# Optimization experiments

Hardware: AMD Instinct MI355X
Metric: run time of the kernel (lower is better)

The kernel has to match this reference:

```python
import jax, jax.numpy as jnp
import numpy as np

# dims
B, N, D, H, L = 2, 4096, 768, 12, 2
DH = D // H          # 64, equals BigBird block_size
BS = 64              # block size
NB = N // BS         # 64 blocks
R = 3                # num_random_blocks
FF = 4 * D
EPS = 1e-12          # BigBird layer_norm_eps


def _ln(x, g, b):
    mu = jnp.mean(x, -1, keepdims=True)
    var = jnp.mean(jnp.square(x - mu), -1, keepdims=True)
    return (x - mu) * jax.lax.rsqrt(var + EPS) * g + b


def _gelu_new(x):
    c = np.sqrt(2.0 / np.pi).astype(np.float32)
    return 0.5 * x * (1.0 + jnp.tanh(c * (x + 0.044715 * x * x * x)))


def _block_sparse_attn(q, k, v, rb):
    # q,k,v: [B,H,N,DH]; rb: [H,NB,R] random block ids (constant)
    scale = 1.0 / np.sqrt(DH).astype(np.float32)
    qb = q.reshape(B, H, NB, BS, DH)
    kb = k.reshape(B, H, NB, BS, DH)
    vb = v.reshape(B, H, NB, BS, DH)
    M = NB - 2
    mids = jnp.arange(1, NB - 1)
    win = jnp.stack([mids - 1, mids, mids + 1], -1)                    # [M,3]
    glb = jnp.broadcast_to(jnp.array([0, NB - 1], jnp.int32), (M, 2))  # [M,2]
    idx = jnp.concatenate([
        jnp.broadcast_to(glb[None], (H, M, 2)),
        jnp.broadcast_to(win[None], (H, M, 3)),
        rb[:, 1:NB - 1, :]], axis=-1)                                  # [H,M,8]
    hh = jnp.arange(H)[:, None, None]
    # gather key/value blocks: [B,H,M,8,BS,DH] -> [B,H,M,512,DH]
    kg = kb[:, hh, idx].reshape(B, H, M, -1, DH)
    vg = vb[:, hh, idx].reshape(B, H, M, -1, DH)
    qm = qb[:, :, 1:NB - 1]                                            # [B,H,M,BS,DH]
    s = jnp.einsum('bhmqd,bhmkd->bhmqk', qm, kg) * scale
    cm = jnp.einsum('bhmqk,bhmkd->bhmqd', jax.nn.softmax(s, -1), vg)
    # first and last query blocks attend globally (full attention)
    qe = jnp.stack([qb[:, :, 0], qb[:, :, -1]], 2)                     # [B,H,2,BS,DH]
    se = jnp.einsum('bheqd,bhkd->bheqk', qe, k) * scale
    ce = jnp.einsum('bheqk,bhkd->bheqd', jax.nn.softmax(se, -1), v)
    out = jnp.concatenate([ce[:, :, :1], cm, ce[:, :, 1:]], axis=2)    # [B,H,NB,BS,DH]
    return out.reshape(B, H, N, DH)


def _forward(inputs_embeds, rand_blocks, pos_emb, tt_emb, emb_ln_g, emb_ln_b,
             Wq, bq, Wk, bk, Wv, bv, Wo, bo, ln1_g, ln1_b,
             Wi, bi, Wd, bd, ln2_g, ln2_b, fc_w, fc_b):
    x = inputs_embeds + pos_emb[None] + tt_emb                         # embeddings (token_type id 0)
    x = _ln(x, emb_ln_g, emb_ln_b)
    for l in range(L):
        q = (x @ Wq[l] + bq[l]).reshape(B, N, H, DH).transpose(0, 2, 1, 3)
        k = (x @ Wk[l] + bk[l]).reshape(B, N, H, DH).transpose(0, 2, 1, 3)
        v = (x @ Wv[l] + bv[l]).reshape(B, N, H, DH).transpose(0, 2, 1, 3)
        ctx = _block_sparse_attn(q, k, v, rand_blocks[l])
        ctx = ctx.transpose(0, 2, 1, 3).reshape(B, N, D)
        a = _ln(x + ctx @ Wo[l] + bo[l], ln1_g[l], ln1_b[l])
        h = _gelu_new(a @ Wi[l] + bi[l])
        x = _ln(a + h @ Wd[l] + bd[l], ln2_g[l], ln2_b[l])
    pooled = jnp.mean(x, axis=1)                                       # [B,D]; dropout is identity at eval
    return (pooled @ fc_w + fc_b).squeeze()                            # [B]


def setup_inputs() -> dict:
    key = jax.random.key(0)
    ks = jax.random.split(key, 24)
    s = 0.02
    nrm = lambda k, shp: jax.random.normal(k, shp, jnp.float32) * s
    return {
        'inputs_embeds': jax.random.normal(ks[0], (B, N, D), jnp.float32),
        'rand_blocks': jax.random.randint(ks[1], (L, H, NB, R), 0, NB, jnp.int32),
        'pos_emb': nrm(ks[2], (N, D)),
        'tt_emb': nrm(ks[3], (D,)),
        'emb_ln_g': jnp.ones((D,), jnp.float32), 'emb_ln_b': jnp.zeros((D,), jnp.float32),
        'Wq': nrm(ks[4], (L, D, D)), 'bq': jnp.zeros((L, D), jnp.float32),
        'Wk': nrm(ks[5], (L, D, D)), 'bk': jnp.zeros((L, D), jnp.float32),
        'Wv': nrm(ks[6], (L, D, D)), 'bv': jnp.zeros((L, D), jnp.float32),
        'Wo': nrm(ks[7], (L, D, D)), 'bo': jnp.zeros((L, D), jnp.float32),
        'ln1_g': jnp.ones((L, D), jnp.float32), 'ln1_b': jnp.zeros((L, D), jnp.float32),
        'Wi': nrm(ks[8], (L, D, FF)), 'bi': jnp.zeros((L, FF), jnp.float32),
        'Wd': nrm(ks[9], (L, FF, D)), 'bd': jnp.zeros((L, D), jnp.float32),
        'ln2_g': jnp.ones((L, D), jnp.float32), 'ln2_b': jnp.zeros((L, D), jnp.float32),
        'fc_w': nrm(ks[10], (D, 1)), 'fc_b': jnp.zeros((1,), jnp.float32),
    }


def reference(inputs_embeds, rand_blocks, pos_emb, tt_emb, emb_ln_g, emb_ln_b,
              Wq, bq, Wk, bk, Wv, bv, Wo, bo, ln1_g, ln1_b,
              Wi, bi, Wd, bd, ln2_g, ln2_b, fc_w, fc_b):
    return _forward(inputs_embeds, rand_blocks, pos_emb, tt_emb, emb_ln_g, emb_ln_b,
                    Wq, bq, Wk, bk, Wv, bv, Wo, bo, ln1_g, ln1_b,
                    Wi, bi, Wd, bd, ln2_g, ln2_b, fc_w, fc_b)
```

## Files before the change

kernel.cpp:

```cpp
#include <hip/hip_runtime.h>
#include <math.h>

#define B_ 2
#define N_ 4096
#define D_ 768
#define H_ 12
#define DH_ 64
#define NB_ 64
#define FF_ 3072
#define LAYERS_ 2
#define ROWS_ (B_ * N_)

typedef __attribute__((ext_vector_type(8))) short s16x8;
typedef __attribute__((ext_vector_type(8))) unsigned short u16x8;
typedef __attribute__((ext_vector_type(4))) float f32x4;

typedef const __attribute__((address_space(1))) unsigned int ga_u32;
typedef __attribute__((address_space(3))) unsigned int lds_u32;

static __device__ __forceinline__ float gelu_fast(float x) {
    float z2 = 1.5957691216057308f * x * (1.0f + 0.044715f * x * x);
    return x * __builtin_amdgcn_rcpf(1.0f + __expf(-z2));
}

static __device__ __forceinline__ unsigned bf16_rne(float f) {
    unsigned u = __float_as_uint(f);
    return (u + 0x7FFFu + ((u >> 16) & 1u)) >> 16;
}
static __device__ __forceinline__ float bfh2f(unsigned short h) {
    return __uint_as_float(((unsigned)h) << 16);
}

__global__ __launch_bounds__(256)
void prep_weights(const float* __restrict__ Wq, const float* __restrict__ Wk,
                  const float* __restrict__ Wv, const float* __restrict__ Wo,
                  const float* __restrict__ Wi, const float* __restrict__ Wd,
                  unsigned short* __restrict__ Wt) {
    const size_t LW = 7077888;
    int bid = blockIdx.x;
    int l = bid / 1728, r = bid % 1728;
    const float* W; unsigned short* T; int K, N, t, nx;
    if (r < 576) {
        int which = r / 144; t = r % 144; nx = 12; K = 768; N = 768;
        W = (which == 0 ? Wq : which == 1 ? Wk : which == 2 ? Wv : Wo) + (size_t)l * D_ * D_;
        T = Wt + l * LW + (size_t)(which < 3 ? which * 768 * 768 : 2304 * 768);
    } else if (r < 1152) {
        t = r - 576; nx = 48; K = 768; N = 3072;
        W = Wi + (size_t)l * D_ * FF_;
        T = Wt + l * LW + (size_t)(2304 * 768 + 768 * 768);
    } else {
        t = r - 1152; nx = 12; K = 3072; N = 768;
        W = Wd + (size_t)l * FF_ * D_;
        T = Wt + l * LW + (size_t)(2304 * 768 + 768 * 768 + 3072 * 768);
    }
    const int bx = t % nx, by = t / nx;
    __shared__ unsigned short tile[64][72];
    const int k0 = by * 64, n0 = bx * 64;
    const int tt = threadIdx.x;
    const int rr = tt >> 2, c0 = (tt & 3) * 16;
    const float* src = W + (size_t)(k0 + rr) * N + n0 + c0;
#pragma unroll
    for (int j = 0; j < 4; ++j) {
        float4 v = *(const float4*)(src + j * 4);
        tile[rr][c0 + j * 4 + 0] = (unsigned short)bf16_rne(v.x);
        tile[rr][c0 + j * 4 + 1] = (unsigned short)bf16_rne(v.y);
        tile[rr][c0 + j * 4 + 2] = (unsigned short)bf16_rne(v.z);
        tile[rr][c0 + j * 4 + 3] = (unsigned short)bf16_rne(v.w);
    }
    __syncthreads();
    const int nr = tt >> 2, kc = (tt & 3) * 16;
    unsigned short* dst = T + (size_t)(n0 + nr) * K + k0 + kc;
    ushort4 o;
#pragma unroll
    for (int j = 0; j < 4; ++j) {
        o.x = tile[kc + j * 4 + 0][nr];
        o.y = tile[kc + j * 4 + 1][nr];
        o.z = tile[kc + j * 4 + 2][nr];
        o.w = tile[kc + j * 4 + 3][nr];
        *(ushort4*)(dst + j * 4) = o;
    }
}

template <int OMODE>
__global__ __launch_bounds__(256)
void gemm_bt(const unsigned short* __restrict__ A, const unsigned short* __restrict__ Bt,
             const float* __restrict__ bias, void* __restrict__ Cv,
             int N, int K, int gelu) {
    __shared__ __align__(16) unsigned short smem[17408];
    const int tid = threadIdx.x, lane = tid & 63, wid = tid >> 6;
    const int bid = blockIdx.x;
    const int row0 = (bid & 63) * 128, col0 = (bid >> 6) * 128;
    const int rh = (wid >> 1) * 64, ch = (wid & 1) * 64;
    const int fr = lane & 15, fq = lane >> 4;
    const int srow = wid * 32 + (lane >> 2);
    const int skoff = ((lane & 3) ^ ((lane >> 3) & 3)) * 8;
    const unsigned short* gA0 = A + (size_t)(row0 + srow) * K + skoff;
    const unsigned short* gA1 = gA0 + (size_t)16 * K;
    const unsigned short* gB0 = Bt + (size_t)(col0 + srow) * K + skoff;
    const unsigned short* gB1 = gB0 + (size_t)16 * K;
    const int rdo = (fq ^ ((fr >> 1) & 3)) * 8;

    f32x4 acc[4][4] = {};
    const int nk = K >> 5;
    {
        unsigned short* s = smem;
        __builtin_amdgcn_global_load_lds((ga_u32*)gA0, (lds_u32*)&s[wid * 1024], 16, 0, 0);
        __builtin_amdgcn_global_load_lds((ga_u32*)gA1, (lds_u32*)&s[wid * 1024 + 512], 16, 0, 0);
        __builtin_amdgcn_global_load_lds((ga_u32*)gB0, (lds_u32*)&s[4096 + wid * 1024], 16, 0, 0);
        __builtin_amdgcn_global_load_lds((ga_u32*)gB1, (lds_u32*)&s[4096 + wid * 1024 + 512], 16, 0, 0);
    }
    for (int kt = 0; kt < nk; ++kt) {
        __syncthreads();
        if (kt + 1 < nk) {
            int k0 = (kt + 1) << 5;
            unsigned short* s = smem + ((kt + 1) & 1) * 8192;
            __builtin_amdgcn_global_load_lds((ga_u32*)(gA0 + k0), (lds_u32*)&s[wid * 1024], 16, 0, 0);
            __builtin_amdgcn_global_load_lds((ga_u32*)(gA1 + k0), (lds_u32*)&s[wid * 1024 + 512], 16, 0, 0);
            __builtin_amdgcn_global_load_lds((ga_u32*)(gB0 + k0), (lds_u32*)&s[4096 + wid * 1024], 16, 0, 0);
            __builtin_amdgcn_global_load_lds((ga_u32*)(gB1 + k0), (lds_u32*)&s[4096 + wid * 1024 + 512], 16, 0, 0);
        }
        const unsigned short* sA = smem + (kt & 1) * 8192;
        const unsigned short* sB = sA + 4096;
        s16x8 af[4], bf[4];
#pragma unroll
        for (int i = 0; i < 4; ++i)
            af[i] = *(const s16x8*)&sA[(rh + 16 * i + fr) * 32 + rdo];
#pragma unroll
        for (int j = 0; j < 4; ++j)
            bf[j] = *(const s16x8*)&sB[(ch + 16 * j + fr) * 32 + rdo];
#pragma unroll
        for (int i = 0; i < 4; ++i)
#pragma unroll
            for (int j = 0; j < 4; ++j)
                acc[i][j] = __builtin_amdgcn_mfma_f32_16x16x32_bf16(af[i], bf[j], acc[i][j], 0, 0, 0);
    }
    if (OMODE == 0) {
#pragma unroll
        for (int j = 0; j < 4; ++j) {
            int col = col0 + ch + 16 * j + fr;
            float bb = bias[col];
#pragma unroll
            for (int i = 0; i < 4; ++i)
#pragma unroll
                for (int r = 0; r < 4; ++r) {
                    int row = row0 + rh + 16 * i + fq * 4 + r;
                    float v = acc[i][j][r] + bb;
                    if (gelu) v = gelu_fast(v);
                    ((float*)Cv)[(size_t)row * N + col] = v;
                }
        }
    } else {
        unsigned short* sC = smem;
        __syncthreads();
#pragma unroll
        for (int j = 0; j < 4; ++j) {
            float bb = bias[col0 + ch + 16 * j + fr];
#pragma unroll
            for (int i = 0; i < 4; ++i)
#pragma unroll
                for (int r = 0; r < 4; ++r) {
                    float v = acc[i][j][r] + bb;
                    if (gelu) v = gelu_fast(v);
                    sC[(rh + 16 * i + fq * 4 + r) * 136 + ch + 16 * j + fr] =
                        (unsigned short)bf16_rne(v);
                }
        }
        __syncthreads();
#pragma unroll
        for (int p = 0; p < 8; ++p) {
            int seg = p * 256 + tid;
            int r = seg >> 4, c8 = (seg & 15) * 8;
            *(u16x8*)&((unsigned short*)Cv)[(size_t)(row0 + r) * N + col0 + c8] =
                *(const u16x8*)&sC[r * 136 + c8];
        }
    }
}

__global__ __launch_bounds__(256)
void gemm_qkv(const unsigned short* __restrict__ A, const unsigned short* __restrict__ Bt,
              const float* __restrict__ bq, const float* __restrict__ bk,
              const float* __restrict__ bv,
              unsigned short* __restrict__ Qh, unsigned short* __restrict__ Kh,
              unsigned short* __restrict__ VT) {
    const int K = D_;
    __shared__ __align__(16) unsigned short smem[17408];
    const int tid = threadIdx.x, lane = tid & 63, wid = tid >> 6;
    const int bid = blockIdx.x;
    const int row0 = (bid & 63) * 128;
    const int bx = bid >> 6;
    const int col0 = bx * 128;
    const int rh = (wid >> 1) * 64, ch = (wid & 1) * 64;
    const int fr = lane & 15, fq = lane >> 4;
    const int srow = wid * 32 + (lane >> 2);
    const int skoff = ((lane & 3) ^ ((lane >> 3) & 3)) * 8;
    const unsigned short* gA0 = A + (size_t)(row0 + srow) * K + skoff;
    const unsigned short* gA1 = gA0 + (size_t)16 * K;
    const unsigned short* gB0 = Bt + (size_t)(col0 + srow) * K + skoff;
    const unsigned short* gB1 = gB0 + (size_t)16 * K;
    const int rdo = (fq ^ ((fr >> 1) & 3)) * 8;

    f32x4 acc[4][4] = {};
    const int nk = K >> 5;
    {
        unsigned short* s = smem;
        __builtin_amdgcn_global_load_lds((ga_u32*)gA0, (lds_u32*)&s[wid * 1024], 16, 0, 0);
        __builtin_amdgcn_global_load_lds((ga_u32*)gA1, (lds_u32*)&s[wid * 1024 + 512], 16, 0, 0);
        __builtin_amdgcn_global_load_lds((ga_u32*)gB0, (lds_u32*)&s[4096 + wid * 1024], 16, 0, 0);
        __builtin_amdgcn_global_load_lds((ga_u32*)gB1, (lds_u32*)&s[4096 + wid * 1024 + 512], 16, 0, 0);
    }
    for (int kt = 0; kt < nk; ++kt) {
        __syncthreads();
        if (kt + 1 < nk) {
            int k0 = (kt + 1) << 5;
            unsigned short* s = smem + ((kt + 1) & 1) * 8192;
            __builtin_amdgcn_global_load_lds((ga_u32*)(gA0 + k0), (lds_u32*)&s[wid * 1024], 16, 0, 0);
            __builtin_amdgcn_global_load_lds((ga_u32*)(gA1 + k0), (lds_u32*)&s[wid * 1024 + 512], 16, 0, 0);
            __builtin_amdgcn_global_load_lds((ga_u32*)(gB0 + k0), (lds_u32*)&s[4096 + wid * 1024], 16, 0, 0);
            __builtin_amdgcn_global_load_lds((ga_u32*)(gB1 + k0), (lds_u32*)&s[4096 + wid * 1024 + 512], 16, 0, 0);
        }
        const unsigned short* sA = smem + (kt & 1) * 8192;
        const unsigned short* sB = sA + 4096;
        s16x8 af[4], bf[4];
#pragma unroll
        for (int i = 0; i < 4; ++i)
            af[i] = *(const s16x8*)&sA[(rh + 16 * i + fr) * 32 + rdo];
#pragma unroll
        for (int j = 0; j < 4; ++j)
            bf[j] = *(const s16x8*)&sB[(ch + 16 * j + fr) * 32 + rdo];
#pragma unroll
        for (int i = 0; i < 4; ++i)
#pragma unroll
            for (int j = 0; j < 4; ++j)
                acc[i][j] = __builtin_amdgcn_mfma_f32_16x16x32_bf16(af[i], bf[j], acc[i][j], 0, 0, 0);
    }
    const int seg = bx / 6;
    const int colbase = col0 - seg * D_;
    const float* bias = (seg == 0) ? bq : (seg == 1) ? bk : bv;
    if (seg == 2) {
#pragma unroll
        for (int j = 0; j < 4; ++j) {
            int col_l = colbase + ch + 16 * j + fr;
            float bb = bias[col_l];
#pragma unroll
            for (int i = 0; i < 4; ++i) {
                int rowbase = row0 + rh + 16 * i + fq * 4;
                ushort4 o;
                o.x = (unsigned short)bf16_rne(acc[i][j][0] + bb);
                o.y = (unsigned short)bf16_rne(acc[i][j][1] + bb);
                o.z = (unsigned short)bf16_rne(acc[i][j][2] + bb);
                o.w = (unsigned short)bf16_rne(acc[i][j][3] + bb);
                *(ushort4*)&VT[(size_t)col_l * ROWS_ + rowbase] = o;
            }
        }
    } else {
        unsigned short* dst = (seg == 0) ? Qh : Kh;
        unsigned short* sC = smem;
        __syncthreads();
#pragma unroll
        for (int j = 0; j < 4; ++j) {
            float bb = bias[colbase + ch + 16 * j + fr];
#pragma unroll
            for (int i = 0; i < 4; ++i)
#pragma unroll
                for (int r = 0; r < 4; ++r)
                    sC[(rh + 16 * i + fq * 4 + r) * 136 + ch + 16 * j + fr] =
                        (unsigned short)bf16_rne(acc[i][j][r] + bb);
        }
        __syncthreads();
#pragma unroll
        for (int p = 0; p < 8; ++p) {
            int seg2 = p * 256 + tid;
            int r = seg2 >> 4, c8 = (seg2 & 15) * 8;
            *(u16x8*)&dst[(size_t)(row0 + r) * D_ + colbase + c8] =
                *(const u16x8*)&sC[r * 136 + c8];
        }
    }
}

__global__ __launch_bounds__(256, 4)
void attn_fused(const unsigned short* __restrict__ Qb, const unsigned short* __restrict__ Kb,
                const unsigned short* __restrict__ VTb, const int* __restrict__ rb,
                unsigned short* __restrict__ ctx, float* __restrict__ scratch) {
    const int MID = B_ * H_ * (NB_ - 2);
    __shared__ __align__(16) unsigned short sQ[64][72];
    __shared__ __align__(16) unsigned short sK[64][72];
    __shared__ __align__(16) unsigned short sVT[64][72];
    __shared__ __align__(16) unsigned short sP[4][16][72];
    __shared__ int sList[16];
    const int tid = threadIdx.x, lane = tid & 63, wid = tid >> 6;
    const int fr = lane & 15, fq = lane >> 4;
    const bool edge = (blockIdx.x >= MID);
    int qb, h, b, nkb, slice = 0;
    if (edge) {
        int e = blockIdx.x - MID;
        int part = e & 3;
        int hh = (e >> 2) % H_;
        int be = (e >> 2) / H_;
        int eb = be & 1;
        b = be >> 1;
        h = hh;
        qb = eb ? (NB_ - 1) : 0;
        nkb = 16;
        slice = ((b * 2 + eb) * H_ + h) * 4 + part;
        if (tid < 16) sList[tid] = part * 16 + tid;
    } else {
        qb = blockIdx.x % (NB_ - 2) + 1;
        h = (blockIdx.x / (NB_ - 2)) % H_;
        b = blockIdx.x / ((NB_ - 2) * H_);
        nkb = 8;
        if (tid < 8) {
            int e;
            if (tid == 0) e = 0;
            else if (tid == 1) e = NB_ - 1;
            else if (tid < 5) e = qb + (tid - 3);
            else e = rb[(h * NB_ + qb) * 3 + (tid - 5)];
            sList[tid] = e;
        }
    }
    const int qrow0 = b * N_ + qb * 64;
    const unsigned short* Qg = Qb + (size_t)qrow0 * D_ + h * 64;
#pragma unroll
    for (int p = 0; p < 2; ++p) {
        int idx = p * 256 + tid;
        int r = idx >> 3, o = (idx & 7) * 8;
        *(u16x8*)&sQ[r][o] = *(const u16x8*)(Qg + (size_t)r * D_ + o);
    }
    f32x4 oacc[4] = {};
    float l_part[4] = {};
    __syncthreads();
    s16x8 aq0 = *(const s16x8*)&sQ[wid * 16 + fr][fq * 8];
    s16x8 aq1 = *(const s16x8*)&sQ[wid * 16 + fr][32 + fq * 8];

    const int stg_r = tid >> 3, stg_o = (tid & 7) * 8;
    u16x8 kreg[2], vreg[2];
    {
        int keyrow0 = b * N_ + sList[0] * 64;
        const unsigned short* Kg = Kb + (size_t)keyrow0 * D_ + h * 64;
        const unsigned short* Vg = VTb + (size_t)(h * 64) * ROWS_ + keyrow0;
#pragma unroll
        for (int p = 0; p < 2; ++p) {
            int r = stg_r + p * 32;
            kreg[p] = *(const u16x8*)(Kg + (size_t)r * D_ + stg_o);
            vreg[p] = *(const u16x8*)(Vg + (size_t)r * ROWS_ + stg_o);
        }
    }

    for (int kb = 0; kb < nkb; ++kb) {
        __syncthreads();
#pragma unroll
        for (int p = 0; p < 2; ++p) {
            int r = stg_r + p * 32;
            *(u16x8*)&sK[r][stg_o] = kreg[p];
            *(u16x8*)&sVT[r][stg_o] = vreg[p];
        }
        __syncthreads();
        if (kb + 1 < nkb) {
            int keyrow0 = b * N_ + sList[kb + 1] * 64;
            const unsigned short* Kg = Kb + (size_t)keyrow0 * D_ + h * 64;
            const unsigned short* Vg = VTb + (size_t)(h * 64) * ROWS_ + keyrow0;
#pragma unroll
            for (int p = 0; p < 2; ++p) {
                int r = stg_r + p * 32;
                kreg[p] = *(const u16x8*)(Kg + (size_t)r * D_ + stg_o);
                vreg[p] = *(const u16x8*)(Vg + (size_t)r * ROWS_ + stg_o);
            }
        }
#pragma unroll
        for (int g = 0; g < 4; ++g) {
            s16x8 bk0 = *(const s16x8*)&sK[g * 16 + fr][fq * 8];
            s16x8 bk1 = *(const s16x8*)&sK[g * 16 + fr][32 + fq * 8];
            f32x4 s = {};
            s = __builtin_amdgcn_mfma_f32_16x16x32_bf16(aq0, bk0, s, 0, 0, 0);
            s = __builtin_amdgcn_mfma_f32_16x16x32_bf16(aq1, bk1, s, 0, 0, 0);
#pragma unroll
            for (int r = 0; r < 4; ++r) {
                float pv = __expf(s[r] * 0.125f);
                l_part[r] += pv;
                sP[wid][fq * 4 + r][g * 16 + fr] = (unsigned short)bf16_rne(pv);
            }
        }
        s16x8 ap0 = *(const s16x8*)&sP[wid][fr][fq * 8];
        s16x8 ap1 = *(const s16x8*)&sP[wid][fr][32 + fq * 8];
#pragma unroll
        for (int g = 0; g < 4; ++g) {
            s16x8 bv0 = *(const s16x8*)&sVT[g * 16 + fr][fq * 8];
            s16x8 bv1 = *(const s16x8*)&sVT[g * 16 + fr][32 + fq * 8];
            oacc[g] = __builtin_amdgcn_mfma_f32_16x16x32_bf16(ap0, bv0, oacc[g], 0, 0, 0);
            oacc[g] = __builtin_amdgcn_mfma_f32_16x16x32_bf16(ap1, bv1, oacc[g], 0, 0, 0);
        }
    }
    float l4[4];
#pragma unroll
    for (int r = 0; r < 4; ++r) {
        float lv = l_part[r];
        lv += __shfl_xor(lv, 1, 64);
        lv += __shfl_xor(lv, 2, 64);
        lv += __shfl_xor(lv, 4, 64);
        lv += __shfl_xor(lv, 8, 64);
        l4[r] = lv;
    }
    if (edge) {
        float* sc = scratch + (size_t)slice * (64 * 64 + 64);
#pragma unroll
        for (int g = 0; g < 4; ++g)
#pragma unroll
            for (int r = 0; r < 4; ++r)
                sc[(wid * 16 + fq * 4 + r) * 64 + g * 16 + fr] = oacc[g][r];
        if (fr == 0) {
#pragma unroll
            for (int r = 0; r < 4; ++r)
                sc[4096 + wid * 16 + fq * 4 + r] = l4[r];
        }
    } else {
        __syncthreads();
#pragma unroll
        for (int g = 0; g < 4; ++g) {
#pragma unroll
            for (int r = 0; r < 4; ++r) {
                float v = oacc[g][r] / l4[r];
                sK[wid * 16 + fq * 4 + r][g * 16 + fr] = (unsigned short)bf16_rne(v);
            }
        }
        __syncthreads();
        unsigned short* Cg = ctx + (size_t)qrow0 * D_ + h * 64;
#pragma unroll
        for (int p = 0; p < 2; ++p) {
            int idx = p * 256 + tid;
            int r = idx >> 3, o = (idx & 7) * 8;
            *(u16x8*)(Cg + (size_t)r * D_ + o) = *(const u16x8*)&sK[r][o];
        }
    }
}

__global__ __launch_bounds__(256)
void edge_combine(const float* __restrict__ scratch, unsigned short* __restrict__ ctx) {
    const int bid = blockIdx.x;
    const int h = bid % H_;
    const int eb = (bid / H_) & 1;
    const int b = bid / (2 * H_);
    const int qb = eb ? (NB_ - 1) : 0;
    const int qrow0 = b * N_ + qb * 64;
    const int slice0 = bid * 4;
    for (int e = threadIdx.x; e < 4096; e += 256) {
        int row = e >> 6, col = e & 63;
        float o = 0.f, l = 0.f;
#pragma unroll
        for (int p = 0; p < 4; ++p) {
            const float* sc = scratch + (size_t)(slice0 + p) * (64 * 64 + 64);
            o += sc[row * 64 + col];
            l += sc[4096 + row];
        }
        ctx[(size_t)(qrow0 + row) * D_ + h * 64 + col] = (unsigned short)bf16_rne(o / l);
    }
}

__global__ __launch_bounds__(256)
void embed_ln_kernel(const float* __restrict__ emb, const float* __restrict__ pos,
                     const float* __restrict__ tt, const float* __restrict__ g,
                     const float* __restrict__ bb, unsigned short* __restrict__ out) {
    const int t = threadIdx.x;
    const int r = t >> 5;
    const int l = t & 31;
    const size_t row = (size_t)blockIdx.x * 8 + r;
    const int n = (int)(row & (N_ - 1));
    const float* ep = emb + row * D_;
    const float* pp = pos + (size_t)n * D_;
    float v[24];
    float s = 0.f;
#pragma unroll
    for (int k = 0; k < 3; ++k) {
        int c0 = k * 256 + l * 8;
        float4 e0 = *(const float4*)(ep + c0);
        float4 e1 = *(const float4*)(ep + c0 + 4);
        float4 p0 = *(const float4*)(pp + c0);
        float4 p1 = *(const float4*)(pp + c0 + 4);
        v[k * 8 + 0] = e0.x + p0.x + tt[c0 + 0];
        v[k * 8 + 1] = e0.y + p0.y + tt[c0 + 1];
        v[k * 8 + 2] = e0.z + p0.z + tt[c0 + 2];
        v[k * 8 + 3] = e0.w + p0.w + tt[c0 + 3];
        v[k * 8 + 4] = e1.x + p1.x + tt[c0 + 4];
        v[k * 8 + 5] = e1.y + p1.y + tt[c0 + 5];
        v[k * 8 + 6] = e1.z + p1.z + tt[c0 + 6];
        v[k * 8 + 7] = e1.w + p1.w + tt[c0 + 7];
#pragma unroll
        for (int j = 0; j < 8; ++j) s += v[k * 8 + j];
    }
#pragma unroll
    for (int off = 16; off > 0; off >>= 1) s += __shfl_xor(s, off, 32);
    const float mu = s * (1.0f / D_);
    float q = 0.f;
#pragma unroll
    for (int i = 0; i < 24; ++i) { float dv = v[i] - mu; q += dv * dv; }
#pragma unroll
    for (int off = 16; off > 0; off >>= 1) q += __shfl_xor(q, off, 32);
    const float rs = rsqrtf(q * (1.0f / D_) + 1e-12f);
    unsigned short* op = out + row * D_;
#pragma unroll
    for (int k = 0; k < 3; ++k) {
        int c0 = k * 256 + l * 8;
        u16x8 o;
#pragma unroll
        for (int j = 0; j < 8; ++j)
            o[j] = (unsigned short)bf16_rne((v[k * 8 + j] - mu) * rs * g[c0 + j] + bb[c0 + j]);
        *(u16x8*)(op + c0) = o;
    }
}

__global__ __launch_bounds__(256)
void add_ln_kernel(const unsigned short* __restrict__ X, const unsigned short* __restrict__ Y,
                   const float* __restrict__ g, const float* __restrict__ bb,
                   unsigned short* __restrict__ out) {
    const int t = threadIdx.x;
    const int r = t >> 5;
    const int l = t & 31;
    const size_t row = (size_t)blockIdx.x * 8 + r;
    const unsigned short* xp = X + row * D_;
    const unsigned short* yp = Y + row * D_;
    float v[24];
    float s = 0.f;
#pragma unroll
    for (int k = 0; k < 3; ++k) {
        u16x8 xv = *(const u16x8*)(xp + k * 256 + l * 8);
        u16x8 yv = *(const u16x8*)(yp + k * 256 + l * 8);
#pragma unroll
        for (int j = 0; j < 8; ++j) {
            float f = bfh2f(xv[j]) + bfh2f(yv[j]);
            v[k * 8 + j] = f;
            s += f;
        }
    }
#pragma unroll
    for (int off = 16; off > 0; off >>= 1) s += __shfl_xor(s, off, 32);
    const float mu = s * (1.0f / D_);
    float q = 0.f;
#pragma unroll
    for (int i = 0; i < 24; ++i) { float dv = v[i] - mu; q += dv * dv; }
#pragma unroll
    for (int off = 16; off > 0; off >>= 1) q += __shfl_xor(q, off, 32);
    const float rs = rsqrtf(q * (1.0f / D_) + 1e-12f);
    unsigned short* op = out + row * D_;
#pragma unroll
    for (int k = 0; k < 3; ++k) {
        int c0 = k * 256 + l * 8;
        u16x8 o;
#pragma unroll
        for (int j = 0; j < 8; ++j)
            o[j] = (unsigned short)bf16_rne((v[k * 8 + j] - mu) * rs * g[c0 + j] + bb[c0 + j]);
        *(u16x8*)(op + c0) = o;
    }
}

__global__ __launch_bounds__(256)
void pool_partial_kernel(const unsigned short* __restrict__ X, float* __restrict__ partial) {
    int blk = blockIdx.x;
    int b = blk >> 6, c = blk & 63;
    int t = threadIdx.x;
#pragma unroll
    for (int i = 0; i < 3; ++i) {
        int d = t + i * 256;
        float s = 0.f;
        for (int n = 0; n < 64; ++n)
            s += bfh2f(X[((size_t)(b * N_ + c * 64 + n)) * D_ + d]);
        partial[(size_t)(b * 64 + c) * D_ + d] = s;
    }
}

__global__ __launch_bounds__(256)
void pool_final_kernel(const float* __restrict__ partial, const float* __restrict__ fcw,
                       const float* __restrict__ fcb, float* __restrict__ out) {
    __shared__ float red[4];
    int t = threadIdx.x;
    for (int b = 0; b < B_; ++b) {
        float s = 0.f;
#pragma unroll
        for (int i = 0; i < 3; ++i) {
            int d = t + i * 256;
            float ps = 0.f;
            for (int c = 0; c < 64; ++c) ps += partial[(size_t)(b * 64 + c) * D_ + d];
            s += ps * (1.0f / N_) * fcw[d];
        }
#pragma unroll
        for (int off = 32; off > 0; off >>= 1) s += __shfl_xor(s, off, 64);
        __syncthreads();
        if ((t & 63) == 0) red[t >> 6] = s;
        __syncthreads();
        if (t == 0) out[b] = red[0] + red[1] + red[2] + red[3] + fcb[0];
    }
}

extern "C" void kernel_launch(void* const* d_in, const int* in_sizes, int n_in,
                              void* d_out, int out_size, void* d_ws, size_t ws_size,
                              hipStream_t stream) {
    (void)in_sizes; (void)n_in; (void)out_size; (void)ws_size;
    const float* emb  = (const float*)d_in[0];
    const int*   rblk = (const int*)d_in[1];
    const float* pos  = (const float*)d_in[2];
    const float* tt   = (const float*)d_in[3];
    const float* elg  = (const float*)d_in[4];
    const float* elb  = (const float*)d_in[5];
    const float* Wq   = (const float*)d_in[6];
    const float* bq   = (const float*)d_in[7];
    const float* Wk   = (const float*)d_in[8];
    const float* bk   = (const float*)d_in[9];
    const float* Wv   = (const float*)d_in[10];
    const float* bv   = (const float*)d_in[11];
    const float* Wo   = (const float*)d_in[12];
    const float* bo   = (const float*)d_in[13];
    const float* ln1g = (const float*)d_in[14];
    const float* ln1b = (const float*)d_in[15];
    const float* Wi   = (const float*)d_in[16];
    const float* bi   = (const float*)d_in[17];
    const float* Wd   = (const float*)d_in[18];
    const float* bd   = (const float*)d_in[19];
    const float* ln2g = (const float*)d_in[20];
    const float* ln2b = (const float*)d_in[21];
    const float* fcw  = (const float*)d_in[22];
    const float* fcb  = (const float*)d_in[23];
    float* outp = (float*)d_out;

    const size_t R = (size_t)ROWS_ * D_;
    float* base = (float*)d_ws;
    unsigned short* Xh  = (unsigned short*)base;
    unsigned short* Abh = (unsigned short*)(base + R / 2);
    unsigned short* Ob  = (unsigned short*)(base + R);
    unsigned short* Qh  = (unsigned short*)(base + 2 * R);
    unsigned short* Kh  = (unsigned short*)(base + 2 * R + R / 2);
    unsigned short* VTh = (unsigned short*)(base + 3 * R);
    unsigned short* Ch  = (unsigned short*)(base + 3 * R + R / 2);
    unsigned short* Hh  = (unsigned short*)(base + 2 * R);
    unsigned short* Wt  = (unsigned short*)(base + 4 * R);
    float* Esc = base + 4 * R + 7077888;
    float* Pp  = Esc + 798720;

    const size_t LW = 7077888;
    const int rows = ROWS_;
    dim3 blk(256);

    prep_weights<<<2 * 1728, blk, 0, stream>>>(Wq, Wk, Wv, Wo, Wi, Wd, Wt);

    embed_ln_kernel<<<rows / 8, blk, 0, stream>>>(emb, pos, tt, elg, elb, Xh);

    for (int l = 0; l < LAYERS_; ++l) {
        const float* bq_l = bq + (size_t)l * D_;
        const float* bk_l = bk + (size_t)l * D_;
        const float* bv_l = bv + (size_t)l * D_;
        const float* bo_l = bo + (size_t)l * D_;
        const float* bi_l = bi + (size_t)l * FF_;
        const float* bd_l = bd + (size_t)l * D_;
        const float* l1g = ln1g + (size_t)l * D_;
        const float* l1b = ln1b + (size_t)l * D_;
        const float* l2g = ln2g + (size_t)l * D_;
        const float* l2b = ln2b + (size_t)l * D_;
        const int* rb_l = rblk + (size_t)l * H_ * NB_ * 3;
        unsigned short* QKVt = Wt + l * LW;
        unsigned short* Ot = QKVt + 2304 * 768;
        unsigned short* It = Ot + 768 * 768;
        unsigned short* Dt = It + 3072 * 768;

        gemm_qkv<<<18 * 64, blk, 0, stream>>>(Xh, QKVt, bq_l, bk_l, bv_l, Qh, Kh, VTh);

        attn_fused<<<B_ * H_ * (NB_ - 2) + B_ * 2 * H_ * 4, blk, 0, stream>>>(
            Qh, Kh, VTh, rb_l, Ch, Esc);
        edge_combine<<<B_ * 2 * H_, blk, 0, stream>>>(Esc, Ch);

        gemm_bt<1><<<6 * 64, blk, 0, stream>>>(Ch, Ot, bo_l, Ob, D_, D_, 0);
        add_ln_kernel<<<rows / 8, blk, 0, stream>>>(Xh, Ob, l1g, l1b, Abh);

        gemm_bt<1><<<24 * 64, blk, 0, stream>>>(Abh, It, bi_l, Hh, FF_, D_, 1);
        gemm_bt<1><<<6 * 64, blk, 0, stream>>>(Hh, Dt, bd_l, Ob, D_, FF_, 0);

        add_ln_kernel<<<rows / 8, blk, 0, stream>>>(Abh, Ob, l2g, l2b, Xh);
    }

    pool_partial_kernel<<<128, blk, 0, stream>>>(Xh, Pp);
    pool_final_kernel<<<1, blk, 0, stream>>>(Pp, fcw, fcb, outp);
}
```

Baseline: 667.1 us.

## Add K=64 double-buffered GEMM for narrow-output projections and stage V transpose via LDS

Adds a new gemm_bt64 kernel that stages 64-wide K tiles into LDS via direct global-to-LDS loads, double-buffered with an XOR swizzle. It replaces the output projection and FFN down-projection GEMMs, which launch only 384 blocks, to cut per-iteration sync overhead and raise the MFMA-to-load ratio. The V-transpose epilogue of the QKV GEMM now goes through LDS so global writes are coalesced 16-byte vectors instead of scattered 8-byte stores. The new GEMM uses 64KB of LDS, which may reduce occupancy.

Measured after the change: 648.8 us. 2.7% less time.

```diff
diff --git a/kernel.cpp b/kernel.cpp
--- a/kernel.cpp
+++ b/kernel.cpp
@@ -173,6 +173,95 @@
             *(u16x8*)&((unsigned short*)Cv)[(size_t)(row0 + r) * N + col0 + c8] =
                 *(const u16x8*)&sC[r * 136 + c8];
         }
+    }
+}
+
+__global__ __launch_bounds__(256)
+void gemm_bt64(const unsigned short* __restrict__ A, const unsigned short* __restrict__ Bt,
+               const float* __restrict__ bias, unsigned short* __restrict__ C,
+               int N, int K, int gelu) {
+    __shared__ __align__(16) unsigned short smem[32768];
+    const int tid = threadIdx.x, lane = tid & 63, wid = tid >> 6;
+    const int bid = blockIdx.x;
+    const int row0 = (bid & 63) * 128, col0 = (bid >> 6) * 128;
+    const int rh = (wid >> 1) * 64, ch = (wid & 1) * 64;
+    const int fr = lane & 15, fq = lane >> 4;
+    const int srow = tid >> 3;
+    const int schunk = tid & 7;
+    const int skoff = (schunk ^ (srow & 7)) * 8;
+    const unsigned short* gA = A + (size_t)row0 * K + skoff;
+    const unsigned short* gB = Bt + (size_t)col0 * K + skoff;
+    const int rx8 = fr & 7;
+    const int rdo0 = (fq ^ rx8) * 8;
+    const int rdo1 = ((4 + fq) ^ rx8) * 8;
+
+    f32x4 acc[4][4] = {};
+    const int nk = K >> 6;
+
+#define STG64(t_, bs_)                                                              \
+    do {                                                                            \
+        _Pragma("unroll") for (int p_ = 0; p_ < 4; ++p_) {                          \
+            __builtin_amdgcn_global_load_lds(                                       \
+                (ga_u32*)(gA + (size_t)(p_ * 32 + srow) * K + ((t_) << 6)),         \
+                (lds_u32*)&smem[(bs_) * 16384 + p_ * 2048 + tid * 8], 16, 0, 0);    \
+            __builtin_amdgcn_global_load_lds(                                       \
+                (ga_u32*)(gB + (size_t)(p_ * 32 + srow) * K + ((t_) << 6)),         \
+                (lds_u32*)&smem[(bs_) * 16384 + 8192 + p_ * 2048 + tid * 8],        \
+                16, 0, 0);                                                          \
+        }                                                                           \
+    } while (0)
+
+    STG64(0, 0);
+    for (int kt = 0; kt < nk; ++kt) {
+        __syncthreads();
+        if (kt + 1 < nk) STG64(kt + 1, (kt + 1) & 1);
+        const unsigned short* sA = smem + (kt & 1) * 16384;
+        const unsigned short* sB = sA + 8192;
+        s16x8 af[4][2], bf[4][2];
+#pragma unroll
+        for (int i = 0; i < 4; ++i) {
+            const unsigned short* p = &sA[(rh + 16 * i + fr) * 64];
+            af[i][0] = *(const s16x8*)(p + rdo0);
+            af[i][1] = *(const s16x8*)(p + rdo1);
+        }
+#pragma unroll
+        for (int j = 0; j < 4; ++j) {
+            const unsigned short* p = &sB[(ch + 16 * j + fr) * 64];
+            bf[j][0] = *(const s16x8*)(p + rdo0);
+            bf[j][1] = *(const s16x8*)(p + rdo1);
+        }
+#pragma unroll
+        for (int i = 0; i < 4; ++i)
+#pragma unroll
+            for (int j = 0; j < 4; ++j) {
+                acc[i][j] = __builtin_amdgcn_mfma_f32_16x16x32_bf16(af[i][0], bf[j][0], acc[i][j], 0, 0, 0);
+                acc[i][j] = __builtin_amdgcn_mfma_f32_16x16x32_bf16(af[i][1], bf[j][1], acc[i][j], 0, 0, 0);
+            }
+    }
+#undef STG64
+
+    unsigned short* sC = smem;
+    __syncthreads();
+#pragma unroll
+    for (int j = 0; j < 4; ++j) {
+        float bb = bias[col0 + ch + 16 * j + fr];
+#pragma unroll
+        for (int i = 0; i < 4; ++i)
+#pragma unroll
+            for (int r = 0; r < 4; ++r) {
+                float v = acc[i][j][r] + bb;
+                if (gelu) v = gelu_fast(v);
+                sC[(rh + 16 * i + fq * 4 + r) * 136 + ch + 16 * j + fr] =
+                    (unsigned short)bf16_rne(v);
+            }
+    }
+    __syncthreads();
+#pragma unroll
+    for (int p = 0; p < 8; ++p) {
+        int seg = p * 256 + tid;
+        int r = seg >> 4, c8 = (seg & 15) * 8;
+        *(u16x8*)&C[(size_t)(row0 + r) * N + col0 + c8] =
+            *(const u16x8*)&sC[r * 136 + c8];
     }
 }
 
@@ -237,20 +326,25 @@
     const int colbase = col0 - seg * D_;
     const float* bias = (seg == 0) ? bq : (seg == 1) ? bk : bv;
     if (seg == 2) {
+        unsigned short* sC = smem;
+        __syncthreads();
 #pragma unroll
         for (int j = 0; j < 4; ++j) {
-            int col_l = colbase + ch + 16 * j + fr;
-            float bb = bias[col_l];
-#pragma unroll
-            for (int i = 0; i < 4; ++i) {
-                int rowbase = row0 + rh + 16 * i + fq * 4;
-                ushort4 o;
-                o.x = (unsigned short)bf16_rne(acc[i][j][0] + bb);
-                o.y = (unsigned short)bf16_rne(acc[i][j][1] + bb);
-                o.z = (unsigned short)bf16_rne(acc[i][j][2] + bb);
-                o.w = (unsigned short)bf16_rne(acc[i][j][3] + bb);
-                *(ushort4*)&VT[(size_t)col_l * ROWS_ + rowbase] = o;
-            }
+            float bb = bias[colbase + ch + 16 * j + fr];
+#pragma unroll
+            for (int i = 0; i < 4; ++i)
+#pragma unroll
+                for (int r = 0; r < 4; ++r)
+                    sC[(ch + 16 * j + fr) * 132 + (rh + 16 * i + fq * 4 + r)] =
+                        (unsigned short)bf16_rne(acc[i][j][r] + bb);
+        }
+        __syncthreads();
+#pragma unroll
+        for (int p = 0; p < 8; ++p) {
+            int idx = p * 256 + tid;
+            int c = idx >> 4, r8 = (idx & 15) * 8;
+            *(u16x8*)&VT[(size_t)(colbase + c) * ROWS_ + row0 + r8] =
+                *(const u16x8*)&sC[c * 132 + r8];
         }
     } else {
         unsigned short* dst = (seg == 0) ? Qh : Kh;
@@ -663,11 +757,11 @@
             Qh, Kh, VTh, rb_l, Ch, Esc);
         edge_combine<<<B_ * 2 * H_, blk, 0, stream>>>(Esc, Ch);
 
-        gemm_bt<1><<<6 * 64, blk, 0, stream>>>(Ch, Ot, bo_l, Ob, D_, D_, 0);
+        gemm_bt64<<<6 * 64, blk, 0, stream>>>(Ch, Ot, bo_l, Ob, D_, D_, 0);
         add_ln_kernel<<<rows / 8, blk, 0, stream>>>(Xh, Ob, l1g, l1b, Abh);
 
         gemm_bt<1><<<24 * 64, blk, 0, stream>>>(Abh, It, bi_l, Hh, FF_, D_, 1);
-        gemm_bt<1><<<6 * 64, blk, 0, stream>>>(Hh, Dt, bd_l, Ob, D_, FF_, 0);
+        gemm_bt64<<<6 * 64, blk, 0, stream>>>(Hh, Dt, bd_l, Ob, D_, FF_, 0);
 
         add_ln_kernel<<<rows / 8, blk, 0, stream>>>(Abh, Ob, l2g, l2b, Xh);
     }
```
